# Kernel optimization log

Hardware: AMD Instinct MI355X
Metric: run time of the kernel (lower is better)

## Reference

```python
import jax, jax.numpy as jnp
import numpy as np

B, C, H, W = 8, 256, 64, 64
EPS = 1e-5


def _mk_conv_bn(key, oc, ic):
    k = jax.random.split(key, 6)
    return dict(
        w=jax.random.normal(k[0], (oc, ic), jnp.float32) * 0.01,  # trunc-normal approx, stddev 0.01
        b=jnp.zeros((oc,), jnp.float32),
        s=jax.random.uniform(k[1], (oc,), jnp.float32, 0.5, 1.5),   # BN scale
        t=jax.random.normal(k[2], (oc,), jnp.float32) * 0.1,        # BN shift
        m=jax.random.normal(k[3], (oc,), jnp.float32) * 0.1,        # BN running mean
        v=jax.random.uniform(k[4], (oc,), jnp.float32, 0.5, 1.5),   # BN running var
    )


def setup_inputs() -> dict:
    key = jax.random.key(0)
    ks = jax.random.split(key, 6)
    d = {"x": jax.random.normal(ks[0], (B, C, H, W), jnp.float32)}
    for i, (oc, ic) in zip([1, 2, 3, 4], [(C // 8, C), (C // 8, C), (C // 2, C), (C, C // 2)]):
        p = _mk_conv_bn(ks[i], oc, ic)
        for name, val in p.items():
            d[f"{name}{i}"] = val
    d["gamma"] = jnp.asarray(0.5, jnp.float32)
    return d


def _cbn(x, w, b, s, t, m, v, relu=True):
    # conv1x1 + BatchNorm(eval) [+ ReLU]; dropout is identity at inference
    y = jnp.einsum('bchw,oc->bohw', x, w) + b[None, :, None, None]
    scale = (s / jnp.sqrt(v + EPS))[None, :, None, None]
    y = (y - m[None, :, None, None]) * scale + t[None, :, None, None]
    return jax.nn.relu(y) if relu else y


def _maxpool2(x):
    b, c, h, w = x.shape
    return x.reshape(b, c, h // 2, 2, w // 2, 2).max(axis=(3, 5))


def reference(x, w1, b1, s1, t1, m1, v1, w2, b2, s2, t2, m2, v2,
              w3, b3, s3, t3, m3, v3, w4, b4, s4, t4, m4, v4, gamma):
    b, c, h, w = x.shape
    f = _maxpool2(_cbn(x, w1, b1, s1, t1, m1, v1))   # (B, C/8, H/2, W/2)
    g = _cbn(x, w2, b2, s2, t2, m2, v2)              # (B, C/8, H, W)
    hh = _maxpool2(_cbn(x, w3, b3, s3, t3, m3, v3))  # (B, C/2, H/2, W/2)
    hw, hw4 = h * w, (h // 2) * (w // 2)
    f = f.reshape(b, c // 8, hw4).transpose(0, 2, 1)  # (B, HW/4, C/8)
    g = g.reshape(b, c // 8, hw)                      # (B, C/8, HW)
    s = jnp.einsum('bnk,bkm->bnm', f, g)              # (B, HW/4, HW)
    beta = jax.nn.softmax(s, axis=1)                  # softmax over dim=1, as in source
    hh = hh.reshape(b, c // 2, hw4)                   # (B, C/2, HW/4)
    o = jnp.einsum('bcn,bnm->bcm', hh, beta).reshape(b, c // 2, h, w)
    out = _cbn(o, w4, b4, s4, t4, m4, v4, relu=False)
    return gamma * out + x
```

## Files before the change

### kernel.cpp

```cpp
#include <hip/hip_runtime.h>
#include <hip/hip_bf16.h>

#define HW   4096
#define HW4  1024
#define EPS  1e-5f
#define SM_SHIFT 20.0f

typedef __attribute__((ext_vector_type(8))) short bf16x8;
typedef __attribute__((ext_vector_type(4))) float f32x4;

__device__ __forceinline__ short f2bs(float f) {
    union { float f; unsigned u; } v; v.f = f;
    unsigned r = v.u + 0x7FFFu + ((v.u >> 16) & 1u);
    return (short)(r >> 16);
}
__device__ __forceinline__ int swz64(int r, int c)  { return (r << 6) + ((c ^ (r & 7))  << 3); }
__device__ __forceinline__ int swz128(int r, int c) { return (r << 7) + ((c ^ (r & 15)) << 3); }
__device__ __forceinline__ int p40(int r, int c)    { return r * 40 + c * 8; }

__global__ __launch_bounds__(256) void conv123pool(
    const float* __restrict__ x,
    const float* __restrict__ w1, const float* __restrict__ b1, const float* __restrict__ s1,
    const float* __restrict__ t1, const float* __restrict__ m1, const float* __restrict__ v1,
    const float* __restrict__ w2, const float* __restrict__ b2, const float* __restrict__ s2,
    const float* __restrict__ t2, const float* __restrict__ m2, const float* __restrict__ v2,
    const float* __restrict__ w3, const float* __restrict__ b3, const float* __restrict__ s3,
    const float* __restrict__ t3, const float* __restrict__ m3, const float* __restrict__ v3,
    const float* __restrict__ w4,
    short* __restrict__ w4T,
    short* __restrict__ gbuf, short* __restrict__ fbufT, short* __restrict__ hhbuf)
{
    __shared__ __align__(16) short Wl[96 * 64];
    __shared__ __align__(16) short Xl[128 * 64];
    __shared__ float alB[96], beB[96];

    const int t = threadIdx.x;
    const int lane = t & 63, wv = t >> 6;
    const int quad = lane >> 4, l16 = lane & 15;
    const int ptile = blockIdx.x;
    const int ocg   = blockIdx.y;
    const int bz    = blockIdx.z;
    const int pBase = ptile * 128;
    const int wcol  = (wv & 1) * 32;
    const int woch  = (wv >> 1) * 48;

    if (ocg == 0 && bz == 0) {
        int idx = (ptile * 256 + t) * 4;
        float4 a = *(const float4*)(w4 + idx);
        short4 o;
        o.x = f2bs(a.x); o.y = f2bs(a.y); o.z = f2bs(a.z); o.w = f2bs(a.w);
        *(short4*)&w4T[idx] = o;
    }

    if (t < 96) {
        int j = ocg * 96 + t;
        float pb, ps, ptv, pm, pv;
        if (j < 32)      { pb = b1[j]; ps = s1[j]; ptv = t1[j]; pm = m1[j]; pv = v1[j]; }
        else if (j < 64) { int c = j - 32; pb = b2[c]; ps = s2[c]; ptv = t2[c]; pm = m2[c]; pv = v2[c]; }
        else             { int c = j - 64; pb = b3[c]; ps = s3[c]; ptv = t3[c]; pm = m3[c]; pv = v3[c]; }
        float al = ps * rsqrtf(pv + EPS);
        alB[t] = al; beB[t] = (pb - pm) * al + ptv;
    }

    const f32x4 fzero = {0.f, 0.f, 0.f, 0.f};
    f32x4 acc[3][4];
    #pragma unroll
    for (int i = 0; i < 3; ++i)
        #pragma unroll
        for (int j = 0; j < 4; ++j) acc[i][j] = fzero;

    const int ptOff0 = wcol, ptOff1 = wcol + 16, ptOff2 = wcol + 64, ptOff3 = wcol + 80;
    const int xp  = t & 127, xk8 = t >> 7;

    for (int k0 = 0; k0 < 256; k0 += 64) {
        #pragma unroll
        for (int i = 0; i < 2; ++i) {
            int idx = t + i * 256;
            if (i == 0 || t < 128) {
                int oc = idx >> 2, kb = (idx & 3) * 16;
                int j = ocg * 96 + oc;
                const float* wp = (j < 32) ? (w1 + j * 256)
                                : (j < 64) ? (w2 + (j - 32) * 256)
                                           : (w3 + (j - 64) * 256);
                wp += k0 + kb;
                float4 a = *(const float4*)(wp);
                float4 b = *(const float4*)(wp + 4);
                float4 c = *(const float4*)(wp + 8);
                float4 d = *(const float4*)(wp + 12);
                bf16x8 lo, hi;
                lo[0]=f2bs(a.x); lo[1]=f2bs(a.y); lo[2]=f2bs(a.z); lo[3]=f2bs(a.w);
                lo[4]=f2bs(b.x); lo[5]=f2bs(b.y); lo[6]=f2bs(b.z); lo[7]=f2bs(b.w);
                hi[0]=f2bs(c.x); hi[1]=f2bs(c.y); hi[2]=f2bs(c.z); hi[3]=f2bs(c.w);
                hi[4]=f2bs(d.x); hi[5]=f2bs(d.y); hi[6]=f2bs(d.z); hi[7]=f2bs(d.w);
                *(bf16x8*)&Wl[swz64(oc, (kb >> 3))]     = lo;
                *(bf16x8*)&Wl[swz64(oc, (kb >> 3) + 1)] = hi;
            }
        }
        {
            const float* xp0 = x + ((size_t)bz * 256 + k0 + xk8 * 32) * HW + pBase + xp;
            float fv[32];
            #pragma unroll
            for (int i = 0; i < 32; ++i) fv[i] = xp0[(size_t)i * HW];
            #pragma unroll
            for (int c = 0; c < 4; ++c) {
                bf16x8 v;
                #pragma unroll
                for (int jj = 0; jj < 8; ++jj) v[jj] = f2bs(fv[c * 8 + jj]);
                *(bf16x8*)&Xl[swz64(xp, xk8 * 4 + c)] = v;
            }
        }
        __syncthreads();
        #pragma unroll
        for (int kk = 0; kk < 2; ++kk) {
            bf16x8 bfr[4];
            bfr[0] = *(const bf16x8*)&Xl[swz64(ptOff0 + l16, kk * 4 + quad)];
            bfr[1] = *(const bf16x8*)&Xl[swz64(ptOff1 + l16, kk * 4 + quad)];
            bfr[2] = *(const bf16x8*)&Xl[swz64(ptOff2 + l16, kk * 4 + quad)];
            bfr[3] = *(const bf16x8*)&Xl[swz64(ptOff3 + l16, kk * 4 + quad)];
            #pragma unroll
            for (int tt = 0; tt < 3; ++tt) {
                bf16x8 afr = *(const bf16x8*)&Wl[swz64(woch + tt * 16 + l16, kk * 4 + quad)];
                #pragma unroll
                for (int pt = 0; pt < 4; ++pt)
                    acc[tt][pt] = __builtin_amdgcn_mfma_f32_16x16x32_bf16(afr, bfr[pt], acc[tt][pt], 0, 0, 0);
            }
        }
        __syncthreads();
    }

    #pragma unroll
    for (int tt = 0; tt < 3; ++tt) {
        #pragma unroll
        for (int r = 0; r < 4; ++r) {
            int ocl = woch + tt * 16 + quad * 4 + r;
            int j = ocg * 96 + ocl;
            float al = alB[ocl], be = beB[ocl];
            float y[4];
            y[0] = fmaxf(acc[tt][0][r] * al + be, 0.f);
            y[1] = fmaxf(acc[tt][1][r] * al + be, 0.f);
            y[2] = fmaxf(acc[tt][2][r] * al + be, 0.f);
            y[3] = fmaxf(acc[tt][3][r] * al + be, 0.f);
            if (j >= 32 && j < 64) {
                size_t base = ((size_t)bz * 32 + (j - 32)) * HW + pBase;
                gbuf[base + ptOff0 + l16] = f2bs(y[0]);
                gbuf[base + ptOff1 + l16] = f2bs(y[1]);
                gbuf[base + ptOff2 + l16] = f2bs(y[2]);
                gbuf[base + ptOff3 + l16] = f2bs(y[3]);
            } else {
                #pragma unroll
                for (int c = 0; c < 2; ++c) {
                    float v  = fmaxf(y[c], y[c + 2]);
                    float po = fmaxf(v, __shfl_xor(v, 1));
                    if ((l16 & 1) == 0) {
                        int col = wcol + c * 16 + l16;
                        int n = ptile * 32 + (col >> 1);
                        if (j < 32) fbufT[((size_t)bz * 1024 + n) * 32 + j] = f2bs(po);
                        else        hhbuf[((size_t)bz * 128 + (j - 64)) * HW4 + n] = f2bs(po);
                    }
                }
            }
        }
    }
}

__global__ __launch_bounds__(256, 2) void attn_conv4(
    const short* __restrict__ gbuf,
    const short* __restrict__ fbufT,
    const short* __restrict__ hhbuf,
    const float* __restrict__ x,
    const short* __restrict__ w4T, const float* __restrict__ b4, const float* __restrict__ s4,
    const float* __restrict__ t4, const float* __restrict__ m4, const float* __restrict__ v4,
    const float* __restrict__ gamma, float* __restrict__ out)
{
    __shared__ __align__(16) short smem[23040];
    __shared__ float alB4[256], beB4[256];
    short* gTl  = smem;
    short* sTl  = smem + 2560;
    short* hhl0 = smem + 6656;
    short* hhl1 = smem + 14848;
    short* o_l  = smem;
    short* Wl4  = smem + 8192;

    const int t = threadIdx.x;
    const int lane = t & 63, wv = t >> 6;
    const int quad = lane >> 4, l16 = lane & 15;
    const int bz = blockIdx.y;
    const int m0 = blockIdx.x * 64;
    const int ms = wv * 16;
    const f32x4 fzero = {0.f, 0.f, 0.f, 0.f};

    {
        float al = s4[t] * rsqrtf(v4[t] + EPS);
        alB4[t] = al; beB4[t] = (b4[t] - m4[t]) * al + t4[t];
    }

    const short* fT = fbufT + (size_t)bz * 1024 * 32;
    const short* hB = hhbuf + (size_t)bz * 128 * HW4;
    const int hrow = t >> 3, hnc = t & 7;

    bf16x8 fr[4], hr[4];
    #pragma unroll
    for (int nt = 0; nt < 4; ++nt)
        fr[nt] = *(const bf16x8*)&fT[(nt * 16 + l16) * 32 + quad * 8];
    #pragma unroll
    for (int i = 0; i < 4; ++i)
        hr[i] = *(const bf16x8*)(hB + (size_t)(i * 32 + hrow) * HW4 + hnc * 8);

    {
        int mm = t & 63, k8 = t >> 6;
        bf16x8 v;
        #pragma unroll
        for (int j = 0; j < 8; ++j)
            v[j] = gbuf[((size_t)bz * 32 + k8 * 8 + j) * HW + m0 + mm];
        *(bf16x8*)&gTl[p40(mm, k8)] = v;
    }
    __syncthreads();
    bf16x8 bg = *(const bf16x8*)&gTl[p40(ms + l16, quad)];

    float psum = 0.f;
    f32x4 oacc[8];
    #pragma unroll
    for (int i = 0; i < 8; ++i) oacc[i] = fzero;

    #pragma unroll 2
    for (int it = 0; it < 16; ++it) {
        const int n0n = ((it + 1) & 15) << 6;
        short* hb = (it & 1) ? hhl1 : hhl0;

        #pragma unroll
        for (int i = 0; i < 4; ++i)
            *(bf16x8*)&hb[swz64(i * 32 + hrow, hnc)] = hr[i];
        #pragma unroll
        for (int i = 0; i < 4; ++i)
            hr[i] = *(const bf16x8*)(hB + (size_t)(i * 32 + hrow) * HW4 + n0n + hnc * 8);
        __syncthreads();

        f32x4 sacc[4];
        #pragma unroll
        for (int nt = 0; nt < 4; ++nt)
            sacc[nt] = __builtin_amdgcn_mfma_f32_16x16x32_bf16(fr[nt], bg, fzero, 0, 0, 0);
        #pragma unroll
        for (int nt = 0; nt < 4; ++nt)
            fr[nt] = *(const bf16x8*)&fT[(n0n + nt * 16 + l16) * 32 + quad * 8];

        #pragma unroll
        for (int nt = 0; nt < 4; ++nt) {
            short4 ev;
            #pragma unroll
            for (int r = 0; r < 4; ++r) {
                float e = __expf(sacc[nt][r] - SM_SHIFT);
                psum += e;
                ((short*)&ev)[r] = f2bs(e);
            }
            int chunk = nt * 2 + (quad >> 1);
            *(short4*)&sTl[swz64(ms + l16, chunk) + (quad & 1) * 4] = ev;
        }

        #pragma unroll
        for (int kk = 0; kk < 2; ++kk) {
            bf16x8 bs = *(const bf16x8*)&sTl[swz64(ms + l16, kk * 4 + quad)];
            #pragma unroll
            for (int ct = 0; ct < 8; ++ct) {
                bf16x8 ah = *(const bf16x8*)&hb[swz64(ct * 16 + l16, kk * 4 + quad)];
                oacc[ct] = __builtin_amdgcn_mfma_f32_16x16x32_bf16(ah, bs, oacc[ct], 0, 0, 0);
            }
        }
    }
    __syncthreads();

    psum += __shfl_xor(psum, 16);
    psum += __shfl_xor(psum, 32);
    {
        float inv = 1.0f / psum;
        int m = ms + l16;
        #pragma unroll
        for (int ct = 0; ct < 8; ++ct) {
            short4 ov;
            #pragma unroll
            for (int r = 0; r < 4; ++r) ((short*)&ov)[r] = f2bs(oacc[ct][r] * inv);
            *(short4*)&o_l[swz128(m, ct * 2 + (quad >> 1)) + (quad & 1) * 4] = ov;
        }
    }

    f32x4 acc4[4][4];
    #pragma unroll
    for (int i = 0; i < 4; ++i)
        #pragma unroll
        for (int j = 0; j < 4; ++j) acc4[i][j] = fzero;

    const int wrow = t >> 2, wcid = t & 3;
    bf16x8 Wr[4];
    #pragma unroll
    for (int g = 0; g < 4; ++g)
        Wr[g] = *(const bf16x8*)(w4T + (g * 64 + wrow) * 128 + wcid * 8);

    #pragma unroll
    for (int k0i = 0; k0i < 4; ++k0i) {
        const int k0 = k0i * 32;
        __syncthreads();
        #pragma unroll
        for (int g = 0; g < 4; ++g)
            *(bf16x8*)&Wl4[p40(g * 64 + wrow, wcid)] = Wr[g];
        if (k0i < 3) {
            #pragma unroll
            for (int g = 0; g < 4; ++g)
                Wr[g] = *(const bf16x8*)(w4T + (g * 64 + wrow) * 128 + k0 + 32 + wcid * 8);
        }
        __syncthreads();
        bf16x8 bfr[4];
        #pragma unroll
        for (int mt = 0; mt < 4; ++mt)
            bfr[mt] = *(const bf16x8*)&o_l[swz128(mt * 16 + l16, (k0 >> 3) + quad)];
        #pragma unroll
        for (int ot = 0; ot < 4; ++ot) {
            bf16x8 afr = *(const bf16x8*)&Wl4[p40(wv * 64 + ot * 16 + l16, quad)];
            #pragma unroll
            for (int mt = 0; mt < 4; ++mt)
                acc4[ot][mt] = __builtin_amdgcn_mfma_f32_16x16x32_bf16(afr, bfr[mt], acc4[ot][mt], 0, 0, 0);
        }
    }

    float gm = gamma[0];
    #pragma unroll
    for (int ot = 0; ot < 4; ++ot) {
        #pragma unroll
        for (int r = 0; r < 4; ++r) {
            int oc = wv * 64 + ot * 16 + quad * 4 + r;
            float al = alB4[oc], be = beB4[oc];
            #pragma unroll
            for (int mt = 0; mt < 4; ++mt) {
                int p = m0 + mt * 16 + l16;
                float y  = acc4[ot][mt][r] * al + be;
                float xo = x[((size_t)bz * 256 + oc) * HW + p];
                out[((size_t)bz * 256 + oc) * HW + p] = gm * y + xo;
            }
        }
    }
}

extern "C" void kernel_launch(void* const* d_in, const int* in_sizes, int n_in,
                              void* d_out, int out_size, void* d_ws, size_t ws_size,
                              hipStream_t stream)
{
    const float* x  = (const float*)d_in[0];
    const float* w1 = (const float*)d_in[1];
    const float* b1 = (const float*)d_in[2];
    const float* s1 = (const float*)d_in[3];
    const float* t1 = (const float*)d_in[4];
    const float* m1 = (const float*)d_in[5];
    const float* v1 = (const float*)d_in[6];
    const float* w2 = (const float*)d_in[7];
    const float* b2 = (const float*)d_in[8];
    const float* s2 = (const float*)d_in[9];
    const float* t2 = (const float*)d_in[10];
    const float* m2 = (const float*)d_in[11];
    const float* v2 = (const float*)d_in[12];
    const float* w3 = (const float*)d_in[13];
    const float* b3 = (const float*)d_in[14];
    const float* s3 = (const float*)d_in[15];
    const float* t3 = (const float*)d_in[16];
    const float* m3 = (const float*)d_in[17];
    const float* v3 = (const float*)d_in[18];
    const float* w4 = (const float*)d_in[19];
    const float* b4 = (const float*)d_in[20];
    const float* s4 = (const float*)d_in[21];
    const float* t4 = (const float*)d_in[22];
    const float* m4 = (const float*)d_in[23];
    const float* v4 = (const float*)d_in[24];
    const float* gm = (const float*)d_in[25];
    float* out = (float*)d_out;

    short* gbuf  = (short*)d_ws;
    short* fbufT = gbuf  + (size_t)8 * 32 * 4096;
    short* hhbuf = fbufT + (size_t)8 * 1024 * 32;
    short* w4T   = hhbuf + (size_t)8 * 128 * 1024;

    conv123pool<<<dim3(32, 2, 8), 256, 0, stream>>>(
        x, w1, b1, s1, t1, m1, v1, w2, b2, s2, t2, m2, v2, w3, b3, s3, t3, m3, v3,
        w4, w4T, gbuf, fbufT, hhbuf);
    attn_conv4<<<dim3(64, 8), 256, 0, stream>>>(
        gbuf, fbufT, hhbuf, x, w4T, b4, s4, t4, m4, v4, gm, out);
}
```

Before: 164.4 us.

## Prefetch x in conv kernel, transpose g buffer, repartition attention PV work

```diff
diff --git a/kernel.cpp b/kernel.cpp
--- a/kernel.cpp
+++ b/kernel.cpp
@@ -6,8 +6,8 @@
 #define EPS  1e-5f
 #define SM_SHIFT 20.0f
 
-typedef __attribute__((ext_vector_type(8))) short bf16x8;
-typedef __attribute__((ext_vector_type(4))) float f32x4;
+typedef __attribute__((ext_vector_type(8)))  short    bf16x8;
+typedef __attribute__((ext_vector_type(4)))  float    f32x4;
 
 __device__ __forceinline__ short f2bs(float f) {
     union { float f; unsigned u; } v; v.f = f;
@@ -28,7 +28,7 @@
     const float* __restrict__ t3, const float* __restrict__ m3, const float* __restrict__ v3,
     const float* __restrict__ w4,
     short* __restrict__ w4T,
-    short* __restrict__ gbuf, short* __restrict__ fbufT, short* __restrict__ hhbuf)
+    short* __restrict__ gbufT, short* __restrict__ fbufT, short* __restrict__ hhbuf)
 {
     __shared__ __align__(16) short Wl[96 * 64];
     __shared__ __align__(16) short Xl[128 * 64];
@@ -71,62 +71,73 @@
 
     const int ptOff0 = wcol, ptOff1 = wcol + 16, ptOff2 = wcol + 64, ptOff3 = wcol + 80;
     const int xp  = t & 127, xk8 = t >> 7;
-
-    for (int k0 = 0; k0 < 256; k0 += 64) {
-        #pragma unroll
-        for (int i = 0; i < 2; ++i) {
-            int idx = t + i * 256;
-            if (i == 0 || t < 128) {
-                int oc = idx >> 2, kb = (idx & 3) * 16;
-                int j = ocg * 96 + oc;
-                const float* wp = (j < 32) ? (w1 + j * 256)
-                                : (j < 64) ? (w2 + (j - 32) * 256)
-                                           : (w3 + (j - 64) * 256);
-                wp += k0 + kb;
-                float4 a = *(const float4*)(wp);
-                float4 b = *(const float4*)(wp + 4);
-                float4 c = *(const float4*)(wp + 8);
-                float4 d = *(const float4*)(wp + 12);
-                bf16x8 lo, hi;
-                lo[0]=f2bs(a.x); lo[1]=f2bs(a.y); lo[2]=f2bs(a.z); lo[3]=f2bs(a.w);
-                lo[4]=f2bs(b.x); lo[5]=f2bs(b.y); lo[6]=f2bs(b.z); lo[7]=f2bs(b.w);
-                hi[0]=f2bs(c.x); hi[1]=f2bs(c.y); hi[2]=f2bs(c.z); hi[3]=f2bs(c.w);
-                hi[4]=f2bs(d.x); hi[5]=f2bs(d.y); hi[6]=f2bs(d.z); hi[7]=f2bs(d.w);
-                *(bf16x8*)&Wl[swz64(oc, (kb >> 3))]     = lo;
-                *(bf16x8*)&Wl[swz64(oc, (kb >> 3) + 1)] = hi;
-            }
-        }
-        {
-            const float* xp0 = x + ((size_t)bz * 256 + k0 + xk8 * 32) * HW + pBase + xp;
-            float fv[32];
-            #pragma unroll
-            for (int i = 0; i < 32; ++i) fv[i] = xp0[(size_t)i * HW];
-            #pragma unroll
-            for (int c = 0; c < 4; ++c) {
-                bf16x8 v;
-                #pragma unroll
-                for (int jj = 0; jj < 8; ++jj) v[jj] = f2bs(fv[c * 8 + jj]);
-                *(bf16x8*)&Xl[swz64(xp, xk8 * 4 + c)] = v;
-            }
-        }
-        __syncthreads();
-        #pragma unroll
-        for (int kk = 0; kk < 2; ++kk) {
-            bf16x8 bfr[4];
-            bfr[0] = *(const bf16x8*)&Xl[swz64(ptOff0 + l16, kk * 4 + quad)];
-            bfr[1] = *(const bf16x8*)&Xl[swz64(ptOff1 + l16, kk * 4 + quad)];
-            bfr[2] = *(const bf16x8*)&Xl[swz64(ptOff2 + l16, kk * 4 + quad)];
-            bfr[3] = *(const bf16x8*)&Xl[swz64(ptOff3 + l16, kk * 4 + quad)];
-            #pragma unroll
-            for (int tt = 0; tt < 3; ++tt) {
-                bf16x8 afr = *(const bf16x8*)&Wl[swz64(woch + tt * 16 + l16, kk * 4 + quad)];
-                #pragma unroll
-                for (int pt = 0; pt < 4; ++pt)
-                    acc[tt][pt] = __builtin_amdgcn_mfma_f32_16x16x32_bf16(afr, bfr[pt], acc[tt][pt], 0, 0, 0);
-            }
-        }
-        __syncthreads();
-    }
+    const float* xBase = x + ((size_t)bz * 256 + xk8 * 32) * HW + pBase + xp;
+
+    float fvA[32], fvB[32];
+    #pragma unroll
+    for (int i = 0; i < 32; ++i) fvA[i] = xBase[(size_t)i * HW];
+
+#define K1_CHUNK(KC, CUR, NXT)                                                        \
+    {                                                                                 \
+        _Pragma("unroll")                                                             \
+        for (int i = 0; i < 2; ++i) {                                                 \
+            int idx = t + i * 256;                                                    \
+            if (i == 0 || t < 128) {                                                  \
+                int oc = idx >> 2, kb = (idx & 3) * 16;                               \
+                int j = ocg * 96 + oc;                                                \
+                const float* wp = (j < 32) ? (w1 + j * 256)                           \
+                                : (j < 64) ? (w2 + (j - 32) * 256)                    \
+                                           : (w3 + (j - 64) * 256);                   \
+                wp += (KC) * 64 + kb;                                                 \
+                float4 a = *(const float4*)(wp);                                      \
+                float4 b = *(const float4*)(wp + 4);                                  \
+                float4 c = *(const float4*)(wp + 8);                                  \
+                float4 d = *(const float4*)(wp + 12);                                 \
+                bf16x8 lo, hi;                                                        \
+                lo[0]=f2bs(a.x); lo[1]=f2bs(a.y); lo[2]=f2bs(a.z); lo[3]=f2bs(a.w);   \
+                lo[4]=f2bs(b.x); lo[5]=f2bs(b.y); lo[6]=f2bs(b.z); lo[7]=f2bs(b.w);   \
+                hi[0]=f2bs(c.x); hi[1]=f2bs(c.y); hi[2]=f2bs(c.z); hi[3]=f2bs(c.w);   \
+                hi[4]=f2bs(d.x); hi[5]=f2bs(d.y); hi[6]=f2bs(d.z); hi[7]=f2bs(d.w);   \
+                *(bf16x8*)&Wl[swz64(oc, (kb >> 3))]     = lo;                         \
+                *(bf16x8*)&Wl[swz64(oc, (kb >> 3) + 1)] = hi;                         \
+            }                                                                         \
+        }                                                                             \
+        if ((KC) < 3) {                                                               \
+            const float* xn = xBase + (size_t)(((KC) + 1) * 64) * HW;                 \
+            _Pragma("unroll")                                                         \
+            for (int i2 = 0; i2 < 32; ++i2) NXT[i2] = xn[(size_t)i2 * HW];            \
+        }                                                                             \
+        _Pragma("unroll")                                                             \
+        for (int c2 = 0; c2 < 4; ++c2) {                                              \
+            bf16x8 v;                                                                 \
+            _Pragma("unroll")                                                         \
+            for (int jj = 0; jj < 8; ++jj) v[jj] = f2bs(CUR[c2 * 8 + jj]);            \
+            *(bf16x8*)&Xl[swz64(xp, xk8 * 4 + c2)] = v;                               \
+        }                                                                             \
+        __syncthreads();                                                              \
+        _Pragma("unroll")                                                             \
+        for (int kk = 0; kk < 2; ++kk) {                                              \
+            bf16x8 bfr[4];                                                            \
+            bfr[0] = *(const bf16x8*)&Xl[swz64(ptOff0 + l16, kk * 4 + quad)];         \
+            bfr[1] = *(const bf16x8*)&Xl[swz64(ptOff1 + l16, kk * 4 + quad)];         \
+            bfr[2] = *(const bf16x8*)&Xl[swz64(ptOff2 + l16, kk * 4 + quad)];         \
+            bfr[3] = *(const bf16x8*)&Xl[swz64(ptOff3 + l16, kk * 4 + quad)];         \
+            _Pragma("unroll")                                                         \
+            for (int tt = 0; tt < 3; ++tt) {                                          \
+                bf16x8 afr = *(const bf16x8*)&Wl[swz64(woch + tt*16 + l16, kk*4 + quad)]; \
+                _Pragma("unroll")                                                     \
+                for (int pt = 0; pt < 4; ++pt)                                        \
+                    acc[tt][pt] = __builtin_amdgcn_mfma_f32_16x16x32_bf16(afr, bfr[pt], acc[tt][pt], 0, 0, 0); \
+            }                                                                         \
+        }                                                                             \
+        __syncthreads();                                                              \
+    }
+
+    K1_CHUNK(0, fvA, fvB)
+    K1_CHUNK(1, fvB, fvA)
+    K1_CHUNK(2, fvA, fvB)
+    K1_CHUNK(3, fvB, fvA)
+#undef K1_CHUNK
 
     #pragma unroll
     for (int tt = 0; tt < 3; ++tt) {
@@ -141,11 +152,12 @@
             y[2] = fmaxf(acc[tt][2][r] * al + be, 0.f);
             y[3] = fmaxf(acc[tt][3][r] * al + be, 0.f);
             if (j >= 32 && j < 64) {
-                size_t base = ((size_t)bz * 32 + (j - 32)) * HW + pBase;
-                gbuf[base + ptOff0 + l16] = f2bs(y[0]);
-                gbuf[base + ptOff1 + l16] = f2bs(y[1]);
-                gbuf[base + ptOff2 + l16] = f2bs(y[2]);
-                gbuf[base + ptOff3 + l16] = f2bs(y[3]);
+                size_t mb = (size_t)bz * 4096 + pBase;
+                int kk = j - 32;
+                gbufT[(mb + ptOff0 + l16) * 32 + kk] = f2bs(y[0]);
+                gbufT[(mb + ptOff1 + l16) * 32 + kk] = f2bs(y[1]);
+                gbufT[(mb + ptOff2 + l16) * 32 + kk] = f2bs(y[2]);
+                gbufT[(mb + ptOff3 + l16) * 32 + kk] = f2bs(y[3]);
             } else {
                 #pragma unroll
                 for (int c = 0; c < 2; ++c) {
@@ -164,7 +176,7 @@
 }
 
 __global__ __launch_bounds__(256, 2) void attn_conv4(
-    const short* __restrict__ gbuf,
+    const short* __restrict__ gbufT,
     const short* __restrict__ fbufT,
     const short* __restrict__ hhbuf,
     const float* __restrict__ x,
@@ -172,12 +184,13 @@
     const float* __restrict__ t4, const float* __restrict__ m4, const float* __restrict__ v4,
     const float* __restrict__ gamma, float* __restrict__ out)
 {
-    __shared__ __align__(16) short smem[23040];
+    __shared__ __align__(16) short smem[24576];
     __shared__ float alB4[256], beB4[256];
-    short* gTl  = smem;
-    short* sTl  = smem + 2560;
-    short* hhl0 = smem + 6656;
-    short* hhl1 = smem + 14848;
+    __shared__ float Zl[64];
+    short* sT0  = smem;
+    short* sT1  = smem + 4096;
+    short* hhl0 = smem + 8192;
+    short* hhl1 = smem + 16384;
     short* o_l  = smem;
     short* Wl4  = smem + 8192;
 
@@ -186,7 +199,6 @@
     const int quad = lane >> 4, l16 = lane & 15;
     const int bz = blockIdx.y;
     const int m0 = blockIdx.x * 64;
-    const int ms = wv * 16;
     const f32x4 fzero = {0.f, 0.f, 0.f, 0.f};
 
     {
@@ -198,6 +210,8 @@
     const short* hB = hhbuf + (size_t)bz * 128 * HW4;
     const int hrow = t >> 3, hnc = t & 7;
 
+    bf16x8 bg = *(const bf16x8*)&gbufT[((size_t)bz * 4096 + m0 + wv * 16 + l16) * 32 + quad * 8];
+
     bf16x8 fr[4], hr[4];
     #pragma unroll
     for (int nt = 0; nt < 4; ++nt)
@@ -206,26 +220,18 @@
     for (int i = 0; i < 4; ++i)
         hr[i] = *(const bf16x8*)(hB + (size_t)(i * 32 + hrow) * HW4 + hnc * 8);
 
-    {
-        int mm = t & 63, k8 = t >> 6;
-        bf16x8 v;
-        #pragma unroll
-        for (int j = 0; j < 8; ++j)
-            v[j] = gbuf[((size_t)bz * 32 + k8 * 8 + j) * HW + m0 + mm];
-        *(bf16x8*)&gTl[p40(mm, k8)] = v;
-    }
-    __syncthreads();
-    bf16x8 bg = *(const bf16x8*)&gTl[p40(ms + l16, quad)];
-
     float psum = 0.f;
-    f32x4 oacc[8];
-    #pragma unroll
-    for (int i = 0; i < 8; ++i) oacc[i] = fzero;
+    f32x4 oacc[2][4];
+    #pragma unroll
+    for (int a = 0; a < 2; ++a)
+        #pragma unroll
+        for (int b = 0; b < 4; ++b) oacc[a][b] = fzero;
 
     #pragma unroll 2
     for (int it = 0; it < 16; ++it) {
         const int n0n = ((it + 1) & 15) << 6;
         short* hb = (it & 1) ? hhl1 : hhl0;
+        short* sT = (it & 1) ? sT1  : sT0;
 
         #pragma unroll
         for (int i = 0; i < 4; ++i)
@@ -233,7 +239,6 @@
         #pragma unroll
         for (int i = 0; i < 4; ++i)
             hr[i] = *(const bf16x8*)(hB + (size_t)(i * 32 + hrow) * HW4 + n0n + hnc * 8);
-        __syncthreads();
 
         f32x4 sacc[4];
         #pragma unroll
@@ -252,33 +257,41 @@
                 psum += e;
                 ((short*)&ev)[r] = f2bs(e);
             }
-            int chunk = nt * 2 + (quad >> 1);
-            *(short4*)&sTl[swz64(ms + l16, chunk) + (quad & 1) * 4] = ev;
-        }
+            *(short4*)&sT[swz64(wv * 16 + l16, nt * 2 + (quad >> 1)) + (quad & 1) * 4] = ev;
+        }
+
+        __syncthreads();
 
         #pragma unroll
         for (int kk = 0; kk < 2; ++kk) {
-            bf16x8 bs = *(const bf16x8*)&sTl[swz64(ms + l16, kk * 4 + quad)];
-            #pragma unroll
-            for (int ct = 0; ct < 8; ++ct) {
-                bf16x8 ah = *(const bf16x8*)&hb[swz64(ct * 16 + l16, kk * 4 + quad)];
-                oacc[ct] = __builtin_amdgcn_mfma_f32_16x16x32_bf16(ah, bs, oacc[ct], 0, 0, 0);
+            bf16x8 ah0 = *(const bf16x8*)&hb[swz64(wv * 32 + l16,      kk * 4 + quad)];
+            bf16x8 ah1 = *(const bf16x8*)&hb[swz64(wv * 32 + 16 + l16, kk * 4 + quad)];
+            bf16x8 bs[4];
+            #pragma unroll
+            for (int mt = 0; mt < 4; ++mt)
+                bs[mt] = *(const bf16x8*)&sT[swz64(mt * 16 + l16, kk * 4 + quad)];
+            #pragma unroll
+            for (int mt = 0; mt < 4; ++mt) {
+                oacc[0][mt] = __builtin_amdgcn_mfma_f32_16x16x32_bf16(ah0, bs[mt], oacc[0][mt], 0, 0, 0);
+                oacc[1][mt] = __builtin_amdgcn_mfma_f32_16x16x32_bf16(ah1, bs[mt], oacc[1][mt], 0, 0, 0);
             }
         }
     }
-    __syncthreads();
 
     psum += __shfl_xor(psum, 16);
     psum += __shfl_xor(psum, 32);
-    {
-        float inv = 1.0f / psum;
-        int m = ms + l16;
-        #pragma unroll
-        for (int ct = 0; ct < 8; ++ct) {
+    if (quad == 0) Zl[wv * 16 + l16] = psum;
+    __syncthreads();
+
+    #pragma unroll
+    for (int mt = 0; mt < 4; ++mt) {
+        float iv = 1.0f / Zl[mt * 16 + l16];
+        #pragma unroll
+        for (int ct2 = 0; ct2 < 2; ++ct2) {
             short4 ov;
             #pragma unroll
-            for (int r = 0; r < 4; ++r) ((short*)&ov)[r] = f2bs(oacc[ct][r] * inv);
-            *(short4*)&o_l[swz128(m, ct * 2 + (quad >> 1)) + (quad & 1) * 4] = ov;
+            for (int r = 0; r < 4; ++r) ((short*)&ov)[r] = f2bs(oacc[ct2][mt][r] * iv);
+            *(short4*)&o_l[swz128(mt * 16 + l16, wv * 4 + ct2 * 2 + (quad >> 1)) + (quad & 1) * 4] = ov;
         }
     }
 
@@ -370,14 +383,14 @@
     const float* gm = (const float*)d_in[25];
     float* out = (float*)d_out;
 
-    short* gbuf  = (short*)d_ws;
-    short* fbufT = gbuf  + (size_t)8 * 32 * 4096;
+    short* gbufT = (short*)d_ws;
+    short* fbufT = gbufT + (size_t)8 * 4096 * 32;
     short* hhbuf = fbufT + (size_t)8 * 1024 * 32;
     short* w4T   = hhbuf + (size_t)8 * 128 * 1024;
 
     conv123pool<<<dim3(32, 2, 8), 256, 0, stream>>>(
         x, w1, b1, s1, t1, m1, v1, w2, b2, s2, t2, m2, v2, w3, b3, s3, t3, m3, v3,
-        w4, w4T, gbuf, fbufT, hhbuf);
+        w4, w4T, gbufT, fbufT, hhbuf);
     attn_conv4<<<dim3(64, 8), 256, 0, stream>>>(
-        gbuf, fbufT, hhbuf, x, w4T, b4, s4, t4, m4, v4, gm, out);
+        gbufT, fbufT, hhbuf, x, w4T, b4, s4, t4, m4, v4, gm, out);
 }
```

Result: faster. 160.3 us (-2.5%).
